# Kernel tuning notes

Measured on AMD Instinct MI355X. Metric: run time of the kernel, lower is better.

Reference implementation:

```python
import jax, jax.numpy as jnp
import numpy as np

N, E = 100_000, 1_600_000
C_IN = C_OUT = 2


def _ln(h, g, b, eps=1e-5):
    mu = h.mean(-1, keepdims=True)
    var = ((h - mu) ** 2).mean(-1, keepdims=True)
    return (h - mu) * jax.lax.rsqrt(var + eps) * g + b


def _radial(x, W1, b1, g1, be1, W2, b2, g2, be2, W3, b3):
    h = jax.nn.relu(_ln(x @ W1 + b1, g1, be1))
    h = jax.nn.relu(_ln(h @ W2 + b2, g2, be2))
    return h @ W3 + b3


def setup_inputs() -> dict:
    key = jax.random.key(0)
    ks = jax.random.split(key, 20)
    inp = {
        "f0": jax.random.normal(ks[0], (N, C_IN, 1), jnp.float32),
        "f1": jax.random.normal(ks[1], (N, C_IN, 3), jnp.float32),
        "dist": jax.random.uniform(ks[2], (E,), jnp.float32),
        "u": jax.random.randint(ks[3], (E,), 0, N),
        "v": jax.random.randint(ks[4], (E,), 0, N),
        "wq": 0.5 * jax.random.normal(ks[5], (2, C_OUT, C_IN), jnp.float32),
        "wj00": jax.random.normal(ks[6], (E, 1, 1, 1), jnp.float32),
        "wj01": jax.random.normal(ks[7], (E, 1, 1, 3), jnp.float32),
        "wj10": jax.random.normal(ks[8], (E, 1, 3, 1), jnp.float32),
        "wj11": jax.random.normal(ks[9], (E, 3, 3, 3), jnp.float32),
        # radial MLP params for the 4 WLayers, index i = 2*l + k
        "rW1": 0.5 * jax.random.normal(ks[10], (4, C_IN + 1, 16), jnp.float32),
        "rb1": jnp.zeros((4, 16), jnp.float32),
        "g1": jnp.ones((4, 16), jnp.float32),
        "be1": jnp.zeros((4, 16), jnp.float32),
        "rW2": 0.3 * jax.random.normal(ks[11], (4, 16, 16), jnp.float32),
        "rb2": jnp.zeros((4, 16), jnp.float32),
        "g2": jnp.ones((4, 16), jnp.float32),
        "be2": jnp.zeros((4, 16), jnp.float32),
        "W3_00": 0.3 * jax.random.normal(ks[12], (16, 4), jnp.float32),
        "b3_00": jnp.zeros((4,), jnp.float32),
        "W3_01": 0.3 * jax.random.normal(ks[13], (16, 4), jnp.float32),
        "b3_01": jnp.zeros((4,), jnp.float32),
        "W3_10": 0.3 * jax.random.normal(ks[14], (16, 4), jnp.float32),
        "b3_10": jnp.zeros((4,), jnp.float32),
        "W3_11": 0.3 * jax.random.normal(ks[15], (16, 12), jnp.float32),
        "b3_11": jnp.zeros((12,), jnp.float32),
    }
    return inp


def reference(f0, f1, dist, u, v, wq, wj00, wj01, wj10, wj11,
              rW1, rb1, g1, be1, rW2, rb2, g2, be2,
              W3_00, b3_00, W3_01, b3_01, W3_10, b3_10, W3_11, b3_11):
    n = f0.shape[0]
    e = u.shape[0]
    # calc_q: [N, c_out, sum(2k+1)=4]
    q = jnp.concatenate([jnp.einsum('oi,nik->nok', wq[0], f0),
                         jnp.einsum('oi,nik->nok', wq[1], f1)], axis=2)
    # per-edge radial input: [dot(f0_src, f0_dst) over rep dim, dist] -> [E, c_in+1]
    vec = jnp.concatenate([jnp.sum(f0[u] * f0[v], axis=2), dist[:, None]], axis=1)
    f_dst = (f0[v], f1[v])  # edges.dst[k]
    wjs = {(0, 0): wj00, (0, 1): wj01, (1, 0): wj10, (1, 1): wj11}
    W3s = {(0, 0): (W3_00, b3_00), (0, 1): (W3_01, b3_01),
           (1, 0): (W3_10, b3_10), (1, 1): (W3_11, b3_11)}
    # calc_k: for each output degree l, sum over input degrees k of
    #   einsum('ejoi,ejlk,eik->eol', R, w_j, f_dst[k])  (fused form of the
    #   original 'ejoi,ejlk->eoilk' then 'eoilk,eik->eol')
    kl = []
    for l in range(2):
        acc = jnp.zeros((e, C_OUT, 2 * l + 1), f0.dtype)
        for k in range(2):
            i = 2 * l + k
            W3, b3 = W3s[(l, k)]
            J = 2 * min(k, l) + 1
            R = _radial(vec, rW1[i], rb1[i], g1[i], be1[i],
                        rW2[i], rb2[i], g2[i], be2[i], W3, b3)
            R = R.reshape(e, J, C_OUT, C_IN)
            acc = acc + jnp.einsum('ejoi,ejlk,eik->eol', R, wjs[(l, k)], f_dst[k])
        kl.append(acc)
    k_feat = jnp.concatenate(kl, axis=2)  # [E, c_out, 4]
    dot = jnp.einsum('eol,eol->e', q[v], k_feat)  # [E]
    # scatter logsumexp over destination nodes, then edge softmax weights
    m = jax.lax.stop_gradient(jax.ops.segment_max(dot, v, num_segments=n))
    m = jnp.where(jnp.isfinite(m), m, 0.0)
    ssum = jax.ops.segment_sum(jnp.exp(dot - m[v]), v, num_segments=n)
    lse = m + jnp.log(ssum)
    return jnp.exp(dot - lse[v])
```

## Files before the change

### kernel.cpp

```cpp
#include <hip/hip_runtime.h>
#include <math.h>


#define TPB 256

typedef float f2 __attribute__((ext_vector_type(2)));
typedef float f4 __attribute__((ext_vector_type(4)));

static __device__ __forceinline__ f2 fma2(f2 a, f2 b, f2 c) {
    return __builtin_elementwise_fma(a, b, c);
}
static __device__ __forceinline__ f2 splat(float x) {
    f2 r;
    r.x = x;
    r.y = x;
    return r;
}
static __device__ __forceinline__ float get16(const f2* h, int c) {
    return (c & 1) ? h[c >> 1].y : h[c >> 1].x;
}

static __device__ __forceinline__ void ln_relu16(f2* h, const float* __restrict__ g,
                                                 const float* __restrict__ be) {
    const f2* g2 = (const f2*)g;
    const f2* be2 = (const f2*)be;
    f2 s = h[0] + h[1] + h[2] + h[3] + h[4] + h[5] + h[6] + h[7];
    const float mu = (s.x + s.y) * 0.0625f;
    const f2 mu2 = splat(mu);
    f2 vs = splat(0.f);
#pragma unroll
    for (int i = 0; i < 8; ++i) {
        f2 d = h[i] - mu2;
        vs = fma2(d, d, vs);
    }
    const float var = (vs.x + vs.y) * 0.0625f;
    const f2 r2 = splat(rsqrtf(var + 1e-5f));
    const f2 zero = splat(0.f);
#pragma unroll
    for (int i = 0; i < 8; ++i) {
        f2 t = (h[i] - mu2) * r2;
        h[i] = __builtin_elementwise_max(fma2(t, g2[i], be2[i]), zero);
    }
}

static __device__ __forceinline__ void radial_h2(
    float v0, float v1, float v2, const float* __restrict__ W1,
    const float* __restrict__ b1, const float* __restrict__ g1,
    const float* __restrict__ be1, const float* __restrict__ W2,
    const float* __restrict__ b2, const float* __restrict__ g2,
    const float* __restrict__ be2, f2* h2) {
    const f2* W1r0 = (const f2*)W1;
    const f2* W1r1 = (const f2*)(W1 + 16);
    const f2* W1r2 = (const f2*)(W1 + 32);
    const f2* b1v = (const f2*)b1;
    const f2 a = splat(v0), b = splat(v1), c = splat(v2);
    f2 h[8];
#pragma unroll
    for (int j = 0; j < 8; ++j)
        h[j] = fma2(a, W1r0[j], fma2(b, W1r1[j], fma2(c, W1r2[j], b1v[j])));
    ln_relu16(h, g1, be1);

    const f2* b2v = (const f2*)b2;
#pragma unroll
    for (int j = 0; j < 8; ++j) h2[j] = b2v[j];
#pragma unroll
    for (int c16 = 0; c16 < 16; ++c16) {
        const f2 hc = splat(get16(h, c16));
        const f2* row = (const f2*)(W2 + c16 * 16);
#pragma unroll
        for (int j = 0; j < 8; ++j) h2[j] = fma2(hc, row[j], h2[j]);
    }
    ln_relu16(h2, g2, be2);
}

static __device__ __forceinline__ void layer3_4(const f2* h2,
                                                const float* __restrict__ W3,
                                                const float* __restrict__ b3,
                                                f2& p0, f2& p1) {
    p0 = *(const f2*)(b3);
    p1 = *(const f2*)(b3 + 2);
#pragma unroll
    for (int c = 0; c < 16; ++c) {
        const f2 hc = splat(get16(h2, c));
        p0 = fma2(hc, *(const f2*)(W3 + c * 4), p0);
        p1 = fma2(hc, *(const f2*)(W3 + c * 4 + 2), p1);
    }
}

__global__ __launch_bounds__(TPB, 2) void edge_kernel(
    const float* __restrict__ f0, const float* __restrict__ f1,
    const float* __restrict__ dist, const int* __restrict__ u,
    const int* __restrict__ v, const float* __restrict__ wq,
    const float* __restrict__ wj00, const float* __restrict__ wj01,
    const float* __restrict__ wj10, const float* __restrict__ wj11,
    const float* __restrict__ rW1, const float* __restrict__ rb1,
    const float* __restrict__ g1, const float* __restrict__ be1,
    const float* __restrict__ rW2, const float* __restrict__ rb2,
    const float* __restrict__ g2, const float* __restrict__ be2,
    const float* __restrict__ W3_00, const float* __restrict__ b3_00,
    const float* __restrict__ W3_01, const float* __restrict__ b3_01,
    const float* __restrict__ W3_10, const float* __restrict__ b3_10,
    const float* __restrict__ W3_11, const float* __restrict__ b3_11,
    float* __restrict__ out, double* __restrict__ ssum, int E) {
    __shared__ __align__(16) float s11[TPB * 27];
    __shared__ __align__(16) float s01[TPB * 3];
    __shared__ __align__(16) float s10[TPB * 3];

    const int tid = threadIdx.x;
    const int base = blockIdx.x * TPB;
    const int nE = (E - base < TPB) ? (E - base) : TPB;

    if (nE == TPB) {
        const f4* s11s = (const f4*)(wj11 + (size_t)base * 27);
        f4* s11d = (f4*)s11;
#pragma unroll 2
        for (int i = tid; i < TPB * 27 / 4; i += TPB) s11d[i] = s11s[i];
        const f4* s01s = (const f4*)(wj01 + (size_t)base * 3);
        const f4* s10s = (const f4*)(wj10 + (size_t)base * 3);
        f4* s01d = (f4*)s01;
        f4* s10d = (f4*)s10;
        for (int i = tid; i < TPB * 3 / 4; i += TPB) {
            s01d[i] = s01s[i];
            s10d[i] = s10s[i];
        }
    } else {
        for (int i = tid; i < nE * 27; i += TPB) s11[i] = wj11[(size_t)base * 27 + i];
        for (int i = tid; i < nE * 3; i += TPB) {
            s01[i] = wj01[(size_t)base * 3 + i];
            s10[i] = wj10[(size_t)base * 3 + i];
        }
    }
    __syncthreads();

    const int e = base + tid;
    if (e >= E) return;

    const float* my11 = s11 + tid * 27;
    const float* my01 = s01 + tid * 3;
    const float* my10 = s10 + tid * 3;

    const int uu = u[e];
    const int vv = v[e];

    const f2 f0u = *(const f2*)(f0 + (size_t)uu * 2);
    const f2 f0v2 = *(const f2*)(f0 + (size_t)vv * 2);
    const float f0v0 = f0v2.x;
    const float f0v1 = f0v2.y;
    const f2 f1a = *(const f2*)(f1 + (size_t)vv * 6);
    const f2 f1b = *(const f2*)(f1 + (size_t)vv * 6 + 2);
    const f2 f1c = *(const f2*)(f1 + (size_t)vv * 6 + 4);
    float f1v[2][3];
    f1v[0][0] = f1a.x; f1v[0][1] = f1a.y; f1v[0][2] = f1b.x;
    f1v[1][0] = f1b.y; f1v[1][1] = f1c.x; f1v[1][2] = f1c.y;

    const float vec0 = f0u.x * f0v0;
    const float vec1 = f0u.y * f0v1;
    const float vec2 = dist[e];

    float acc0[2] = {0.f, 0.f};
    float acc1[2][3] = {{0.f, 0.f, 0.f}, {0.f, 0.f, 0.f}};

    {
        f2 h2[8];
        radial_h2(vec0, vec1, vec2, rW1 + 0 * 48, rb1 + 0 * 16, g1 + 0 * 16,
                  be1 + 0 * 16, rW2 + 0 * 256, rb2 + 0 * 16, g2 + 0 * 16,
                  be2 + 0 * 16, h2);
        f2 p0, p1;
        layer3_4(h2, W3_00, b3_00, p0, p1);
        const float w = wj00[e];
        acc0[0] += w * (p0.x * f0v0 + p0.y * f0v1);
        acc0[1] += w * (p1.x * f0v0 + p1.y * f0v1);
    }
    {
        f2 h2[8];
        radial_h2(vec0, vec1, vec2, rW1 + 1 * 48, rb1 + 1 * 16, g1 + 1 * 16,
                  be1 + 1 * 16, rW2 + 1 * 256, rb2 + 1 * 16, g2 + 1 * 16,
                  be2 + 1 * 16, h2);
        f2 p0, p1;
        layer3_4(h2, W3_01, b3_01, p0, p1);
        const float w0 = my01[0];
        const float w1 = my01[1];
        const float w2 = my01[2];
        const float s0 = w0 * f1v[0][0] + w1 * f1v[0][1] + w2 * f1v[0][2];
        const float s1 = w0 * f1v[1][0] + w1 * f1v[1][1] + w2 * f1v[1][2];
        acc0[0] += p0.x * s0 + p0.y * s1;
        acc0[1] += p1.x * s0 + p1.y * s1;
    }
    {
        f2 h2[8];
        radial_h2(vec0, vec1, vec2, rW1 + 2 * 48, rb1 + 2 * 16, g1 + 2 * 16,
                  be1 + 2 * 16, rW2 + 2 * 256, rb2 + 2 * 16, g2 + 2 * 16,
                  be2 + 2 * 16, h2);
        f2 p0, p1;
        layer3_4(h2, W3_10, b3_10, p0, p1);
        const float t0 = p0.x * f0v0 + p0.y * f0v1;
        const float t1 = p1.x * f0v0 + p1.y * f0v1;
#pragma unroll
        for (int m = 0; m < 3; ++m) {
            const float w = my10[m];
            acc1[0][m] += w * t0;
            acc1[1][m] += w * t1;
        }
    }
    {
        f2 h2[8];
        radial_h2(vec0, vec1, vec2, rW1 + 3 * 48, rb1 + 3 * 16, g1 + 3 * 16,
                  be1 + 3 * 16, rW2 + 3 * 256, rb2 + 3 * 16, g2 + 3 * 16,
                  be2 + 3 * 16, h2);
#pragma unroll
        for (int j = 0; j < 3; ++j) {
            f2 p0 = *(const f2*)(b3_11 + j * 4);
            f2 p1 = *(const f2*)(b3_11 + j * 4 + 2);
#pragma unroll
            for (int c = 0; c < 16; ++c) {
                const f2 hc = splat(get16(h2, c));
                p0 = fma2(hc, *(const f2*)(W3_11 + c * 12 + j * 4), p0);
                p1 = fma2(hc, *(const f2*)(W3_11 + c * 12 + j * 4 + 2), p1);
            }
#pragma unroll
            for (int m = 0; m < 3; ++m) {
                const float w0 = my11[j * 9 + m * 3 + 0];
                const float w1 = my11[j * 9 + m * 3 + 1];
                const float w2 = my11[j * 9 + m * 3 + 2];
                const float B0 =
                    w0 * f1v[0][0] + w1 * f1v[0][1] + w2 * f1v[0][2];
                const float B1 =
                    w0 * f1v[1][0] + w1 * f1v[1][1] + w2 * f1v[1][2];
                acc1[0][m] += p0.x * B0 + p0.y * B1;
                acc1[1][m] += p1.x * B0 + p1.y * B1;
            }
        }
    }

    float dot = 0.f;
    {
        const float q00 = wq[0] * f0v0 + wq[1] * f0v1;
        const float q01 = wq[2] * f0v0 + wq[3] * f0v1;
        dot += q00 * acc0[0] + q01 * acc0[1];
#pragma unroll
        for (int m = 0; m < 3; ++m) {
            const float q1m0 = wq[4] * f1v[0][m] + wq[5] * f1v[1][m];
            const float q1m1 = wq[6] * f1v[0][m] + wq[7] * f1v[1][m];
            dot += q1m0 * acc1[0][m] + q1m1 * acc1[1][m];
        }
    }

    out[e] = dot;
    atomicAdd(&ssum[vv], exp((double)dot));
}

__global__ void norm_kernel(float* __restrict__ out, const int* __restrict__ v,
                            const double* __restrict__ ssum, int E) {
    int e = blockIdx.x * blockDim.x + threadIdx.x;
    if (e >= E) return;
    const double t = exp((double)out[e]);
    out[e] = (float)(t / ssum[v[e]]);
}

extern "C" void kernel_launch(void* const* d_in, const int* in_sizes, int n_in,
                              void* d_out, int out_size, void* d_ws,
                              size_t ws_size, hipStream_t stream) {
    const float* f0 = (const float*)d_in[0];
    const float* f1 = (const float*)d_in[1];
    const float* dist = (const float*)d_in[2];
    const int* u = (const int*)d_in[3];
    const int* v = (const int*)d_in[4];
    const float* wq = (const float*)d_in[5];
    const float* wj00 = (const float*)d_in[6];
    const float* wj01 = (const float*)d_in[7];
    const float* wj10 = (const float*)d_in[8];
    const float* wj11 = (const float*)d_in[9];
    const float* rW1 = (const float*)d_in[10];
    const float* rb1 = (const float*)d_in[11];
    const float* g1 = (const float*)d_in[12];
    const float* be1 = (const float*)d_in[13];
    const float* rW2 = (const float*)d_in[14];
    const float* rb2 = (const float*)d_in[15];
    const float* g2 = (const float*)d_in[16];
    const float* be2 = (const float*)d_in[17];
    const float* W3_00 = (const float*)d_in[18];
    const float* b3_00 = (const float*)d_in[19];
    const float* W3_01 = (const float*)d_in[20];
    const float* b3_01 = (const float*)d_in[21];
    const float* W3_10 = (const float*)d_in[22];
    const float* b3_10 = (const float*)d_in[23];
    const float* W3_11 = (const float*)d_in[24];
    const float* b3_11 = (const float*)d_in[25];

    const int N = in_sizes[0] / 2;
    const int E = in_sizes[2];

    double* ssum = (double*)d_ws;
    float* out = (float*)d_out;

    const int ge = (E + TPB - 1) / TPB;

    hipMemsetAsync(ssum, 0, (size_t)N * sizeof(double), stream);
    edge_kernel<<<ge, TPB, 0, stream>>>(
        f0, f1, dist, u, v, wq, wj00, wj01, wj10, wj11, rW1, rb1, g1, be1, rW2,
        rb2, g2, be2, W3_00, b3_00, W3_01, b3_01, W3_10, b3_10, W3_11, b3_11,
        out, ssum, E);
    norm_kernel<<<ge, TPB, 0, stream>>>(out, v, ssum, E);
}
```

Baseline: 422.2 us.

## Split the four radial MLP branches across wavefronts, one edge per lane

Each block now handles 64 edges with four wavefronts, and each wavefront evaluates one of the four radial MLP branches for every edge. Partial dot products are combined through shared memory before the atomic logsumexp accumulation. This cuts per-thread serial work and register pressure, which the launch bound raising occupancy to 6 relies on, and lets more independent work hide latency. The cost is redundant per-edge gathers in every wavefront, uneven branch cost (the l=1,k=1 branch is heavier), and an extra block-wide sync.

```diff
diff --git a/kernel.cpp b/kernel.cpp
--- a/kernel.cpp
+++ b/kernel.cpp
@@ -3,6 +3,7 @@
 
 
 #define TPB 256
+#define EPB 64
 
 typedef float f2 __attribute__((ext_vector_type(2)));
 typedef float f4 __attribute__((ext_vector_type(4)));
@@ -87,7 +88,7 @@
     }
 }
 
-__global__ __launch_bounds__(TPB, 2) void edge_kernel(
+__global__ __launch_bounds__(TPB, 6) void edge_kernel(
     const float* __restrict__ f0, const float* __restrict__ f1,
     const float* __restrict__ dist, const int* __restrict__ u,
     const int* __restrict__ v, const float* __restrict__ wq,
@@ -102,26 +103,24 @@
     const float* __restrict__ W3_10, const float* __restrict__ b3_10,
     const float* __restrict__ W3_11, const float* __restrict__ b3_11,
     float* __restrict__ out, double* __restrict__ ssum, int E) {
-    __shared__ __align__(16) float s11[TPB * 27];
-    __shared__ __align__(16) float s01[TPB * 3];
-    __shared__ __align__(16) float s10[TPB * 3];
+    __shared__ __align__(16) float s11[EPB * 27];
+    __shared__ __align__(16) float s01[EPB * 3];
+    __shared__ __align__(16) float s10[EPB * 3];
+    __shared__ float pdot[4][EPB];
 
     const int tid = threadIdx.x;
-    const int base = blockIdx.x * TPB;
-    const int nE = (E - base < TPB) ? (E - base) : TPB;
-
-    if (nE == TPB) {
+    const int base = blockIdx.x * EPB;
+    const int rem = E - base;
+    const int nE = (rem < EPB) ? rem : EPB;
+
+    if (nE == EPB) {
         const f4* s11s = (const f4*)(wj11 + (size_t)base * 27);
         f4* s11d = (f4*)s11;
 #pragma unroll 2
-        for (int i = tid; i < TPB * 27 / 4; i += TPB) s11d[i] = s11s[i];
-        const f4* s01s = (const f4*)(wj01 + (size_t)base * 3);
-        const f4* s10s = (const f4*)(wj10 + (size_t)base * 3);
-        f4* s01d = (f4*)s01;
-        f4* s10d = (f4*)s10;
-        for (int i = tid; i < TPB * 3 / 4; i += TPB) {
-            s01d[i] = s01s[i];
-            s10d[i] = s10s[i];
+        for (int i = tid; i < EPB * 27 / 4; i += TPB) s11d[i] = s11s[i];
+        if (tid < EPB * 3 / 4) {
+            ((f4*)s01)[tid] = ((const f4*)(wj01 + (size_t)base * 3))[tid];
+            ((f4*)s10)[tid] = ((const f4*)(wj10 + (size_t)base * 3))[tid];
         }
     } else {
         for (int i = tid; i < nE * 27; i += TPB) s11[i] = wj11[(size_t)base * 27 + i];
@@ -132,121 +131,119 @@
     }
     __syncthreads();
 
-    const int e = base + tid;
-    if (e >= E) return;
-
-    const float* my11 = s11 + tid * 27;
-    const float* my01 = s01 + tid * 3;
-    const float* my10 = s10 + tid * 3;
-
-    const int uu = u[e];
-    const int vv = v[e];
-
-    const f2 f0u = *(const f2*)(f0 + (size_t)uu * 2);
-    const f2 f0v2 = *(const f2*)(f0 + (size_t)vv * 2);
-    const float f0v0 = f0v2.x;
-    const float f0v1 = f0v2.y;
-    const f2 f1a = *(const f2*)(f1 + (size_t)vv * 6);
-    const f2 f1b = *(const f2*)(f1 + (size_t)vv * 6 + 2);
-    const f2 f1c = *(const f2*)(f1 + (size_t)vv * 6 + 4);
-    float f1v[2][3];
-    f1v[0][0] = f1a.x; f1v[0][1] = f1a.y; f1v[0][2] = f1b.x;
-    f1v[1][0] = f1b.y; f1v[1][1] = f1c.x; f1v[1][2] = f1c.y;
-
-    const float vec0 = f0u.x * f0v0;
-    const float vec1 = f0u.y * f0v1;
-    const float vec2 = dist[e];
-
-    float acc0[2] = {0.f, 0.f};
-    float acc1[2][3] = {{0.f, 0.f, 0.f}, {0.f, 0.f, 0.f}};
-
-    {
+    const int lane = tid & 63;
+    const int w = __builtin_amdgcn_readfirstlane(tid >> 6);
+    const int e = base + lane;
+
+    float dotw = 0.f;
+    int vv = 0;
+    if (e < E) {
+        const int uu = u[e];
+        vv = v[e];
+
+        const f2 f0u = *(const f2*)(f0 + (size_t)uu * 2);
+        const f2 f0v2 = *(const f2*)(f0 + (size_t)vv * 2);
+        const float f0v0 = f0v2.x;
+        const float f0v1 = f0v2.y;
+
+        float f1v[2][3];
+        if (w != 0) {
+            const f2 f1a = *(const f2*)(f1 + (size_t)vv * 6);
+            const f2 f1b = *(const f2*)(f1 + (size_t)vv * 6 + 2);
+            const f2 f1c = *(const f2*)(f1 + (size_t)vv * 6 + 4);
+            f1v[0][0] = f1a.x; f1v[0][1] = f1a.y; f1v[0][2] = f1b.x;
+            f1v[1][0] = f1b.y; f1v[1][1] = f1c.x; f1v[1][2] = f1c.y;
+        }
+
+        const float vec0 = f0u.x * f0v0;
+        const float vec1 = f0u.y * f0v1;
+        const float vec2 = dist[e];
+
         f2 h2[8];
-        radial_h2(vec0, vec1, vec2, rW1 + 0 * 48, rb1 + 0 * 16, g1 + 0 * 16,
-                  be1 + 0 * 16, rW2 + 0 * 256, rb2 + 0 * 16, g2 + 0 * 16,
-                  be2 + 0 * 16, h2);
-        f2 p0, p1;
-        layer3_4(h2, W3_00, b3_00, p0, p1);
-        const float w = wj00[e];
-        acc0[0] += w * (p0.x * f0v0 + p0.y * f0v1);
-        acc0[1] += w * (p1.x * f0v0 + p1.y * f0v1);
-    }
-    {
-        f2 h2[8];
-        radial_h2(vec0, vec1, vec2, rW1 + 1 * 48, rb1 + 1 * 16, g1 + 1 * 16,
-                  be1 + 1 * 16, rW2 + 1 * 256, rb2 + 1 * 16, g2 + 1 * 16,
-                  be2 + 1 * 16, h2);
-        f2 p0, p1;
-        layer3_4(h2, W3_01, b3_01, p0, p1);
-        const float w0 = my01[0];
-        const float w1 = my01[1];
-        const float w2 = my01[2];
-        const float s0 = w0 * f1v[0][0] + w1 * f1v[0][1] + w2 * f1v[0][2];
-        const float s1 = w0 * f1v[1][0] + w1 * f1v[1][1] + w2 * f1v[1][2];
-        acc0[0] += p0.x * s0 + p0.y * s1;
-        acc0[1] += p1.x * s0 + p1.y * s1;
-    }
-    {
-        f2 h2[8];
-        radial_h2(vec0, vec1, vec2, rW1 + 2 * 48, rb1 + 2 * 16, g1 + 2 * 16,
-                  be1 + 2 * 16, rW2 + 2 * 256, rb2 + 2 * 16, g2 + 2 * 16,
-                  be2 + 2 * 16, h2);
-        f2 p0, p1;
-        layer3_4(h2, W3_10, b3_10, p0, p1);
-        const float t0 = p0.x * f0v0 + p0.y * f0v1;
-        const float t1 = p1.x * f0v0 + p1.y * f0v1;
-#pragma unroll
-        for (int m = 0; m < 3; ++m) {
-            const float w = my10[m];
-            acc1[0][m] += w * t0;
-            acc1[1][m] += w * t1;
-        }
-    }
-    {
-        f2 h2[8];
-        radial_h2(vec0, vec1, vec2, rW1 + 3 * 48, rb1 + 3 * 16, g1 + 3 * 16,
-                  be1 + 3 * 16, rW2 + 3 * 256, rb2 + 3 * 16, g2 + 3 * 16,
-                  be2 + 3 * 16, h2);
-#pragma unroll
-        for (int j = 0; j < 3; ++j) {
-            f2 p0 = *(const f2*)(b3_11 + j * 4);
-            f2 p1 = *(const f2*)(b3_11 + j * 4 + 2);
-#pragma unroll
-            for (int c = 0; c < 16; ++c) {
-                const f2 hc = splat(get16(h2, c));
-                p0 = fma2(hc, *(const f2*)(W3_11 + c * 12 + j * 4), p0);
-                p1 = fma2(hc, *(const f2*)(W3_11 + c * 12 + j * 4 + 2), p1);
+        radial_h2(vec0, vec1, vec2, rW1 + w * 48, rb1 + w * 16, g1 + w * 16,
+                  be1 + w * 16, rW2 + w * 256, rb2 + w * 16, g2 + w * 16,
+                  be2 + w * 16, h2);
+
+        if (w == 0) {
+            f2 p0, p1;
+            layer3_4(h2, W3_00, b3_00, p0, p1);
+            const float wj = wj00[e];
+            const float a0 = wj * (p0.x * f0v0 + p0.y * f0v1);
+            const float a1 = wj * (p1.x * f0v0 + p1.y * f0v1);
+            const float q00 = wq[0] * f0v0 + wq[1] * f0v1;
+            const float q01 = wq[2] * f0v0 + wq[3] * f0v1;
+            dotw = q00 * a0 + q01 * a1;
+        } else if (w == 1) {
+            f2 p0, p1;
+            layer3_4(h2, W3_01, b3_01, p0, p1);
+            const float* my01 = s01 + lane * 3;
+            const float w0 = my01[0];
+            const float w1 = my01[1];
+            const float w2 = my01[2];
+            const float s0 = w0 * f1v[0][0] + w1 * f1v[0][1] + w2 * f1v[0][2];
+            const float s1 = w0 * f1v[1][0] + w1 * f1v[1][1] + w2 * f1v[1][2];
+            const float a0 = p0.x * s0 + p0.y * s1;
+            const float a1 = p1.x * s0 + p1.y * s1;
+            const float q00 = wq[0] * f0v0 + wq[1] * f0v1;
+            const float q01 = wq[2] * f0v0 + wq[3] * f0v1;
+            dotw = q00 * a0 + q01 * a1;
+        } else if (w == 2) {
+            f2 p0, p1;
+            layer3_4(h2, W3_10, b3_10, p0, p1);
+            const float t0 = p0.x * f0v0 + p0.y * f0v1;
+            const float t1 = p1.x * f0v0 + p1.y * f0v1;
+            const float* my10 = s10 + lane * 3;
+#pragma unroll
+            for (int m = 0; m < 3; ++m) {
+                const float wm = my10[m];
+                const float q1m0 = wq[4] * f1v[0][m] + wq[5] * f1v[1][m];
+                const float q1m1 = wq[6] * f1v[0][m] + wq[7] * f1v[1][m];
+                dotw += q1m0 * (wm * t0) + q1m1 * (wm * t1);
             }
+        } else {
+            const float* my11 = s11 + lane * 27;
+            float acc1[2][3] = {{0.f, 0.f, 0.f}, {0.f, 0.f, 0.f}};
+#pragma unroll
+            for (int j = 0; j < 3; ++j) {
+                f2 p0 = *(const f2*)(b3_11 + j * 4);
+                f2 p1 = *(const f2*)(b3_11 + j * 4 + 2);
+#pragma unroll
+                for (int c = 0; c < 16; ++c) {
+                    const f2 hc = splat(get16(h2, c));
+                    p0 = fma2(hc, *(const f2*)(W3_11 + c * 12 + j * 4), p0);
+                    p1 = fma2(hc, *(const f2*)(W3_11 + c * 12 + j * 4 + 2), p1);
+                }
+#pragma unroll
+                for (int m = 0; m < 3; ++m) {
+                    const float w0 = my11[j * 9 + m * 3 + 0];
+                    const float w1 = my11[j * 9 + m * 3 + 1];
+                    const float w2 = my11[j * 9 + m * 3 + 2];
+                    const float B0 =
+                        w0 * f1v[0][0] + w1 * f1v[0][1] + w2 * f1v[0][2];
+                    const float B1 =
+                        w0 * f1v[1][0] + w1 * f1v[1][1] + w2 * f1v[1][2];
+                    acc1[0][m] += p0.x * B0 + p0.y * B1;
+                    acc1[1][m] += p1.x * B0 + p1.y * B1;
+                }
+            }
 #pragma unroll
             for (int m = 0; m < 3; ++m) {
-                const float w0 = my11[j * 9 + m * 3 + 0];
-                const float w1 = my11[j * 9 + m * 3 + 1];
-                const float w2 = my11[j * 9 + m * 3 + 2];
-                const float B0 =
-                    w0 * f1v[0][0] + w1 * f1v[0][1] + w2 * f1v[0][2];
-                const float B1 =
-                    w0 * f1v[1][0] + w1 * f1v[1][1] + w2 * f1v[1][2];
-                acc1[0][m] += p0.x * B0 + p0.y * B1;
-                acc1[1][m] += p1.x * B0 + p1.y * B1;
+                const float q1m0 = wq[4] * f1v[0][m] + wq[5] * f1v[1][m];
+                const float q1m1 = wq[6] * f1v[0][m] + wq[7] * f1v[1][m];
+                dotw += q1m0 * acc1[0][m] + q1m1 * acc1[1][m];
             }
         }
     }
 
-    float dot = 0.f;
-    {
-        const float q00 = wq[0] * f0v0 + wq[1] * f0v1;
-        const float q01 = wq[2] * f0v0 + wq[3] * f0v1;
-        dot += q00 * acc0[0] + q01 * acc0[1];
-#pragma unroll
-        for (int m = 0; m < 3; ++m) {
-            const float q1m0 = wq[4] * f1v[0][m] + wq[5] * f1v[1][m];
-            const float q1m1 = wq[6] * f1v[0][m] + wq[7] * f1v[1][m];
-            dot += q1m0 * acc1[0][m] + q1m1 * acc1[1][m];
-        }
-    }
-
-    out[e] = dot;
-    atomicAdd(&ssum[vv], exp((double)dot));
+    pdot[w][lane] = dotw;
+    __syncthreads();
+
+    if (w == 0 && e < E) {
+        const float dot =
+            pdot[0][lane] + pdot[1][lane] + pdot[2][lane] + pdot[3][lane];
+        out[e] = dot;
+        atomicAdd(&ssum[vv], exp((double)dot));
+    }
 }
 
 __global__ void norm_kernel(float* __restrict__ out, const int* __restrict__ v,
@@ -293,12 +290,12 @@
     double* ssum = (double*)d_ws;
     float* out = (float*)d_out;
 
-    const int ge = (E + TPB - 1) / TPB;
-
     hipMemsetAsync(ssum, 0, (size_t)N * sizeof(double), stream);
+    const int ge = (E + EPB - 1) / EPB;
     edge_kernel<<<ge, TPB, 0, stream>>>(
         f0, f1, dist, u, v, wq, wj00, wj01, wj10, wj11, rW1, rb1, g1, be1, rW2,
         rb2, g2, be2, W3_00, b3_00, W3_01, b3_01, W3_10, b3_10, W3_11, b3_11,
         out, ssum, E);
-    norm_kernel<<<ge, TPB, 0, stream>>>(out, v, ssum, E);
-}
+    const int gn = (E + TPB - 1) / TPB;
+    norm_kernel<<<gn, TPB, 0, stream>>>(out, v, ssum, E);
+}
```

New measurement: 427.5 us. About the same (+1.3%).
